# Kernel optimization log

Hardware: AMD Instinct MI355X
Metric: run time of the kernel (lower is better)

The kernel has to match this reference:

```python
import jax, jax.numpy as jnp
import numpy as np

N = 100000
IN_F, C1, C2, C3, OUT_F = 64, 64, 64, 64, 8


def setup_inputs() -> dict:
    key = jax.random.key(0)
    ks = jax.random.split(key, 12)
    x = jax.random.normal(ks[0], (N, IN_F), dtype=jnp.float32)
    edge_index = jax.random.randint(ks[1], (2, 1600000), 0, N, dtype=jnp.int64)

    def lin(kw, kb, fi, fo):
        s = 1.0 / np.sqrt(fi)
        W = jax.random.uniform(kw, (fi, fo), jnp.float32, -s, s)
        b = jax.random.uniform(kb, (fo,), jnp.float32, -s, s)
        return W, b

    W1, b1 = lin(ks[2], ks[3], IN_F, C1)
    W2, b2 = lin(ks[4], ks[5], C1, C2)
    W3, b3 = lin(ks[6], ks[7], C2, C3)
    Wl, bl = lin(ks[8], ks[9], C3, OUT_F)
    return {"x": x, "edge_index": edge_index, "W1": W1, "b1": b1,
            "W2": W2, "b2": b2, "W3": W3, "b3": b3, "Wl": Wl, "bl": bl}


def _gcn_norm(edge_index, n):
    # add self loops, compute symmetric normalization D^-1/2 A D^-1/2
    loops = jnp.arange(n, dtype=edge_index.dtype)
    src = jnp.concatenate([edge_index[0], loops])
    dst = jnp.concatenate([edge_index[1], loops])
    deg = jax.ops.segment_sum(jnp.ones_like(dst, dtype=jnp.float32), dst, num_segments=n)
    dis = jnp.where(deg > 0, jax.lax.rsqrt(deg), 0.0)
    norm = dis[src] * dis[dst]  # [E+N]
    return src, dst, norm


def _gcn_layer(h, W, b, src, dst, norm, n):
    h = h @ W                                   # [N, Fout] small GEMM
    msg = h[src] * norm[:, None]                # gather + scale, [E+N, Fout]
    agg = jax.ops.segment_sum(msg, dst, num_segments=n)  # scatter-add
    return agg + b


def reference(x, edge_index, W1, b1, W2, b2, W3, b3, Wl, bl):
    n = x.shape[0]
    src, dst, norm = _gcn_norm(edge_index, n)
    h = jax.nn.relu(_gcn_layer(x, W1, b1, src, dst, norm, n))
    h = jax.nn.relu(_gcn_layer(h, W2, b2, src, dst, norm, n))
    h = jax.nn.relu(_gcn_layer(h, W3, b3, src, dst, norm, n))
    return h @ Wl + bl
```

## Files before the change

kernel.cpp:

```cpp
#include <hip/hip_runtime.h>
#include <hip/hip_fp16.h>

#define F 64
#define CHUNK 2048
#define BN 512
#define BSHIFT 9
#define CAP 20480

typedef int v4i __attribute__((ext_vector_type(4)));

__device__ __forceinline__ float rlane(float v, int l) {
    return __uint_as_float(__builtin_amdgcn_readlane(__float_as_uint(v), l));
}

__global__ __launch_bounds__(256) void k_blkcnt(const int* __restrict__ dst,
                                                int* __restrict__ blkcnt,
                                                int E, int NB, int NBKT) {
    __shared__ int lcnt[256];
    int b = blockIdx.x, t = threadIdx.x;
    lcnt[t] = 0;
    __syncthreads();
    int e0 = b * CHUNK;
#pragma unroll
    for (int k = 0; k < 8; ++k) {
        int e = e0 + t + k * 256;
        if (e < E) {
            int d = __builtin_nontemporal_load(&dst[e]);
            atomicAdd(&lcnt[d >> BSHIFT], 1);
        }
    }
    __syncthreads();
    if (t < NBKT) blkcnt[t * NB + b] = lcnt[t];
}

__global__ __launch_bounds__(256) void k_bktscan(const int* __restrict__ blkcnt,
                                                 int* __restrict__ blkoff,
                                                 int* __restrict__ bkttot, int NB) {
    __shared__ int s[256];
    __shared__ int running;
    int seg = blockIdx.x;
    int t = threadIdx.x;
    if (t == 0) running = 0;
    __syncthreads();
    for (int base = 0; base < NB; base += 256) {
        int i = base + t;
        int v = (i < NB) ? blkcnt[seg * NB + i] : 0;
        s[t] = v;
        __syncthreads();
        for (int off = 1; off < 256; off <<= 1) {
            int x = (t >= off) ? s[t - off] : 0;
            __syncthreads();
            s[t] += x;
            __syncthreads();
        }
        int rbase = running;
        if (i < NB) blkoff[seg * NB + i] = rbase + s[t] - v;
        int ctot = s[255];
        __syncthreads();
        if (t == 0) running = rbase + ctot;
        __syncthreads();
    }
    if (t == 0) bkttot[seg] = running;
}

__global__ void k_sb(const int* __restrict__ bkttot, int* __restrict__ sb, int NBKT) {
    __shared__ int s[256];
    int t = threadIdx.x;
    int v = (t < NBKT) ? bkttot[t] : 0;
    s[t] = v;
    __syncthreads();
    for (int off = 1; off < 256; off <<= 1) {
        int x = (t >= off) ? s[t - off] : 0;
        __syncthreads();
        s[t] += x;
        __syncthreads();
    }
    if (t < NBKT) sb[t] = s[t] - v;
    if (t == NBKT - 1) sb[NBKT] = s[t];
}

__global__ __launch_bounds__(256) void k_stage2(const int* __restrict__ src,
                                                const int* __restrict__ dst,
                                                const int* __restrict__ blkoff,
                                                const int* __restrict__ sb,
                                                uint2* __restrict__ stage,
                                                int E, int NB, int NBKT) {
    __shared__ int lcnt[256];
    __shared__ int lbase[257];
    __shared__ int obase[256];
    __shared__ int s[256];
    __shared__ uint2 rec[CHUNK];
    __shared__ unsigned char binof[CHUNK];
    int b = blockIdx.x, t = threadIdx.x;
    lcnt[t] = 0;
    __syncthreads();
    int e0 = b * CHUNK;
    int myseg[8], myrank[8];
    uint2 myrec[8];
#pragma unroll
    for (int k = 0; k < 8; ++k) {
        int e = e0 + t + k * 256;
        myseg[k] = -1;
        if (e < E) {
            int d = __builtin_nontemporal_load(&dst[e]);
            int sv = __builtin_nontemporal_load(&src[e]);
            int sg = d >> BSHIFT;
            myseg[k] = sg;
            myrank[k] = atomicAdd(&lcnt[sg], 1);
            myrec[k] = make_uint2((unsigned)d, (unsigned)sv);
        }
    }
    __syncthreads();
    int v = lcnt[t];
    s[t] = v;
    __syncthreads();
    for (int off = 1; off < 256; off <<= 1) {
        int x = (t >= off) ? s[t - off] : 0;
        __syncthreads();
        s[t] += x;
        __syncthreads();
    }
    lbase[t] = s[t] - v;
    if (t == 255) lbase[256] = s[255];
    obase[t] = (t < NBKT) ? sb[t] + blkoff[t * NB + b] : 0;
    __syncthreads();
#pragma unroll
    for (int k = 0; k < 8; ++k) {
        if (myseg[k] >= 0) {
            int p = lbase[myseg[k]] + myrank[k];
            rec[p] = myrec[k];
            binof[p] = (unsigned char)myseg[k];
        }
    }
    __syncthreads();
    int tot = lbase[256];
    for (int j = t; j < tot; j += 256) {
        int sg = binof[j];
        stage[obase[sg] + (j - lbase[sg])] = rec[j];
    }
}

__global__ __launch_bounds__(1024) void k_bincount(const uint2* __restrict__ stage,
                                                   const int* __restrict__ sb,
                                                   int* __restrict__ count, int n) {
    __shared__ int lc[BN];
    int bkt = blockIdx.x, t = threadIdx.x;
    int nb0 = bkt << BSHIFT;
    for (int q = t; q < BN; q += 1024) lc[q] = 0;
    __syncthreads();
    int r0 = sb[bkt], r1 = sb[bkt + 1];
    for (int j = r0 + t; j < r1; j += 1024) {
        uint2 r = stage[j];
        atomicAdd(&lc[(int)r.x - nb0], 1);
    }
    __syncthreads();
    for (int q = t; q < BN; q += 1024) {
        int node = nb0 + q;
        if (node < n) count[node] = lc[q];
    }
}

__global__ void k_reduce(const int* __restrict__ c, int* __restrict__ bsum, int n) {
    __shared__ int s[256];
    int t = threadIdx.x;
    int i = blockIdx.x * 256 + t;
    s[t] = (i < n) ? ((c[i] + 3) & ~3) : 0;
    __syncthreads();
    for (int off = 128; off > 0; off >>= 1) {
        if (t < off) s[t] += s[t + off];
        __syncthreads();
    }
    if (t == 0) bsum[blockIdx.x] = s[0];
}

__global__ void k_scan_bsum(int* bs, int nb) {
    __shared__ int s[512];
    int t = threadIdx.x;
    int v = (t < nb) ? bs[t] : 0;
    s[t] = v;
    __syncthreads();
    for (int off = 1; off < 512; off <<= 1) {
        int x = (t >= off) ? s[t - off] : 0;
        __syncthreads();
        s[t] += x;
        __syncthreads();
    }
    if (t < nb) bs[t] = s[t] - v;
}

__global__ void k_scan_write(const int* __restrict__ c, const int* __restrict__ boff,
                             int* __restrict__ row_start, float* __restrict__ dis, int n) {
    __shared__ int s[256];
    int t = threadIdx.x;
    int i = blockIdx.x * 256 + t;
    int cv = (i < n) ? c[i] : 0;
    int v = (cv + 3) & ~3;
    if (i >= n) v = 0;
    s[t] = v;
    __syncthreads();
    for (int off = 1; off < 256; off <<= 1) {
        int x = (t >= off) ? s[t - off] : 0;
        __syncthreads();
        s[t] += x;
        __syncthreads();
    }
    if (i <= n) {
        row_start[i] = s[t] - v + boff[blockIdx.x];
        if (i < n) dis[i] = rsqrtf((float)(cv + 1));
    }
}

__global__ __launch_bounds__(256) void k_binfill(const uint2* __restrict__ stage,
                                                 const int* __restrict__ sb,
                                                 const int* __restrict__ row_start,
                                                 int* __restrict__ csr, int n) {
    __shared__ int lcur[BN];
    __shared__ int buf[CAP];
    int bkt = blockIdx.x, t = threadIdx.x;
    int nb0 = bkt << BSHIFT;
    int nend = min(nb0 + BN, n);
    int w0 = row_start[nb0];
    int w1 = row_start[nend];
    int wlen = w1 - w0;
    for (int j = t; j < wlen && j < CAP; j += 256) buf[j] = n;
    for (int q = t; q < BN; q += 256) {
        int node = nb0 + q;
        lcur[q] = (node < nend) ? row_start[node] - w0 : 0;
    }
    __syncthreads();
    int r0 = sb[bkt], r1 = sb[bkt + 1];
    for (int j = r0 + t; j < r1; j += 256) {
        uint2 r = stage[j];
        int p = atomicAdd(&lcur[(int)r.x - nb0], 1);
        if (p < CAP) buf[p] = (int)r.y;
    }
    __syncthreads();
    for (int j = t; j < wlen && j < CAP; j += 256) csr[w0 + j] = buf[j];
}

__global__ void k_prep(const float4* __restrict__ x4, const float* __restrict__ dis,
                       uint2* __restrict__ hs, uint2* __restrict__ hs2, int n) {
    int i = blockIdx.x * blockDim.x + threadIdx.x;
    int tot = (n + 1) * 16;
    if (i < tot) {
        int row = i >> 4;
        float dv = 0.0f;
        float4 v = make_float4(0.f, 0.f, 0.f, 0.f);
        if (row < n) { dv = dis[row]; v = x4[i]; }
        __half2 h01 = __floats2half2_rn(dv * v.x, dv * v.y);
        __half2 h23 = __floats2half2_rn(dv * v.z, dv * v.w);
        uint2 u;
        u.x = *(unsigned*)&h01;
        u.y = *(unsigned*)&h23;
        hs[i] = u;
    } else if (i < tot + 16) {
        hs2[(size_t)n * 16 + (i - tot)] = make_uint2(0u, 0u);
    }
}

__device__ __forceinline__ void h4acc(uint2 u, float* t) {
    float2 fa = __half22float2(*(__half2*)&u.x);
    float2 fb = __half22float2(*(__half2*)&u.y);
    t[0] += fa.x; t[1] += fa.y; t[2] += fb.x; t[3] += fb.y;
}

__global__ __launch_bounds__(256) void k_layer(const __half* __restrict__ hin,
                                               const float* __restrict__ W,
                                               const float* __restrict__ b,
                                               const int* __restrict__ row_start,
                                               const int* __restrict__ csr,
                                               const float* __restrict__ dis,
                                               __half* __restrict__ hout,
                                               int n, int scale_out) {
    __shared__ float Ws[F * F];
    int tid = threadIdx.x;
#pragma unroll
    for (int i = 0; i < 16; ++i) Ws[tid + i * 256] = W[tid + i * 256];
    __syncthreads();
    int lane = tid & 63;
    int g = lane >> 4;
    int sub = lane & 15;
    int r0 = (blockIdx.x * 4 + (tid >> 6)) * 4;
    if (r0 >= n) return;

    int s0 = row_start[r0];
    int s1 = row_start[r0 + 1];
    int s2 = row_start[r0 + 2];
    int s3 = row_start[r0 + 3];
    int s4 = row_start[r0 + 4];

    float a0[4] = {0, 0, 0, 0};
    float a1[4] = {0, 0, 0, 0};
    float a2[4] = {0, 0, 0, 0};
    float a3[4] = {0, 0, 0, 0};

    const v4i* csr4 = (const v4i*)csr;
    const uint2* h2 = (const uint2*)hin;
    int B0 = s0 >> 2, B4 = s4 >> 2;

    auto ldidx = [&](int bb) -> v4i {
        int mybb = bb + g;
        bool valid = mybb < B4;
        v4i qq = __builtin_nontemporal_load(csr4 + (valid ? mybb : B0));
        if (!valid) { qq.x = n; qq.y = n; qq.z = n; qq.w = n; }
        return qq;
    };

    if (B0 < B4) {
        v4i qcur = ldidx(B0);
        v4i qnxt = (B0 + 4 < B4) ? ldidx(B0 + 4) : qcur;
        uint2 Gc0 = h2[((size_t)qcur.x << 4) + sub];
        uint2 Gc1 = h2[((size_t)qcur.y << 4) + sub];
        uint2 Gc2 = h2[((size_t)qcur.z << 4) + sub];
        uint2 Gc3 = h2[((size_t)qcur.w << 4) + sub];

        for (int bb = B0; bb < B4; bb += 4) {
            bool hasn = bb + 4 < B4;
            uint2 Gn0, Gn1, Gn2, Gn3;
            if (hasn) {
                Gn0 = h2[((size_t)qnxt.x << 4) + sub];
                Gn1 = h2[((size_t)qnxt.y << 4) + sub];
                Gn2 = h2[((size_t)qnxt.z << 4) + sub];
                Gn3 = h2[((size_t)qnxt.w << 4) + sub];
            }
            v4i qn2 = (bb + 8 < B4) ? ldidx(bb + 8) : qnxt;

            int slot = (bb + g) << 2;
            int r = (slot >= s1) + ((slot >= s2) + (slot >= s3));
            float t[4] = {0, 0, 0, 0};
            h4acc(Gc0, t); h4acc(Gc1, t); h4acc(Gc2, t); h4acc(Gc3, t);
            float m0 = (r == 0) ? 1.0f : 0.0f;
            float m1 = (r == 1) ? 1.0f : 0.0f;
            float m2 = (r == 2) ? 1.0f : 0.0f;
            float m3 = (r == 3) ? 1.0f : 0.0f;
#pragma unroll
            for (int m = 0; m < 4; ++m) {
                a0[m] = fmaf(m0, t[m], a0[m]);
                a1[m] = fmaf(m1, t[m], a1[m]);
                a2[m] = fmaf(m2, t[m], a2[m]);
                a3[m] = fmaf(m3, t[m], a3[m]);
            }
            qnxt = qn2;
            if (hasn) { Gc0 = Gn0; Gc1 = Gn1; Gc2 = Gn2; Gc3 = Gn3; }
        }
    }

#pragma unroll
    for (int m = 0; m < 4; ++m) {
        a0[m] += __shfl_xor(a0[m], 16); a0[m] += __shfl_xor(a0[m], 32);
        a1[m] += __shfl_xor(a1[m], 16); a1[m] += __shfl_xor(a1[m], 32);
        a2[m] += __shfl_xor(a2[m], 16); a2[m] += __shfl_xor(a2[m], 32);
        a3[m] += __shfl_xor(a3[m], 16); a3[m] += __shfl_xor(a3[m], 32);
    }

    {
        uint2 u0 = h2[((size_t)(r0 + 0) << 4) + sub];
        uint2 u1 = h2[((size_t)(r0 + 1) << 4) + sub];
        uint2 u2 = h2[((size_t)(r0 + 2) << 4) + sub];
        uint2 u3 = h2[((size_t)(r0 + 3) << 4) + sub];
        h4acc(u0, a0); h4acc(u1, a1); h4acc(u2, a2); h4acc(u3, a3);
    }
    float d0 = dis[r0 + 0], d1 = dis[r0 + 1], d2 = dis[r0 + 2], d3 = dis[r0 + 3];
#pragma unroll
    for (int m = 0; m < 4; ++m) {
        a0[m] *= d0; a1[m] *= d1; a2[m] *= d2; a3[m] *= d3;
    }

    float bb_ = b[lane];
    float y0 = bb_, y1 = bb_, y2 = bb_, y3 = bb_;
#pragma unroll
    for (int a = 0; a < 16; ++a) {
#pragma unroll
        for (int m = 0; m < 4; ++m) {
            float w = Ws[(((a << 2) + m) << 6) + lane];
            y0 = fmaf(rlane(a0[m], a), w, y0);
            y1 = fmaf(rlane(a1[m], a), w, y1);
            y2 = fmaf(rlane(a2[m], a), w, y2);
            y3 = fmaf(rlane(a3[m], a), w, y3);
        }
    }
    y0 = fmaxf(y0, 0.0f);
    y1 = fmaxf(y1, 0.0f);
    y2 = fmaxf(y2, 0.0f);
    y3 = fmaxf(y3, 0.0f);
    if (scale_out) { y0 *= d0; y1 *= d1; y2 *= d2; y3 *= d3; }
    hout[((size_t)(r0 + 0) << 6) + lane] = __float2half(y0);
    hout[((size_t)(r0 + 1) << 6) + lane] = __float2half(y1);
    hout[((size_t)(r0 + 2) << 6) + lane] = __float2half(y2);
    hout[((size_t)(r0 + 3) << 6) + lane] = __float2half(y3);
}

__global__ __launch_bounds__(256) void k_final(const __half* __restrict__ h,
                                               const float* __restrict__ Wl,
                                               const float* __restrict__ bl,
                                               float* __restrict__ out, int n) {
    __shared__ float Ws[F * 8];
    __shared__ float bs[8];
    int tid = threadIdx.x;
    Ws[tid] = Wl[tid];
    Ws[tid + 256] = Wl[tid + 256];
    if (tid < 8) bs[tid] = bl[tid];
    __syncthreads();
    int idx = blockIdx.x * 256 + tid;
    if (idx >= n * 8) return;
    int row = idx >> 3;
    int o = idx & 7;
    const __half* hr = h + (size_t)row * F;
    float acc = bs[o];
#pragma unroll
    for (int k = 0; k < F; ++k) acc = fmaf(__half2float(hr[k]), Ws[k * 8 + o], acc);
    out[idx] = acc;
}

extern "C" void kernel_launch(void* const* d_in, const int* in_sizes, int n_in,
                              void* d_out, int out_size, void* d_ws, size_t ws_size,
                              hipStream_t stream) {
    const float* x  = (const float*)d_in[0];
    const int*   ei = (const int*)d_in[1];
    const float* W1 = (const float*)d_in[2];
    const float* b1 = (const float*)d_in[3];
    const float* W2 = (const float*)d_in[4];
    const float* b2 = (const float*)d_in[5];
    const float* W3 = (const float*)d_in[6];
    const float* b3 = (const float*)d_in[7];
    const float* Wl = (const float*)d_in[8];
    const float* bl = (const float*)d_in[9];
    float* out = (float*)d_out;

    int n = in_sizes[0] / F;
    int E = in_sizes[1] / 2;
    const int* src = ei;
    const int* dst = ei + E;

    int np   = (n + 256) & ~255;
    int nb   = (np + 255) / 256;
    int cap  = E + 3 * n + 64;
    int NB   = (E + CHUNK - 1) / CHUNK;
    int NBKT = (n + BN - 1) >> BSHIFT;

    int*    count     = (int*)d_ws;
    int*    row_start = count + np;
    int*    bsum      = row_start + np;
    int*    blkcnt    = bsum + 512;
    int*    blkoff    = blkcnt + 256 * NB;
    int*    bkttot    = blkoff + 256 * NB;
    int*    sb        = bkttot + 256;
    float*  dis       = (float*)(sb + 272);
    uint2*  stage     = (uint2*)(dis + np);
    int*    csr       = (int*)(stage + E);
    __half* buf1      = (__half*)(csr + ((cap + 3) & ~3));
    __half* buf2      = buf1 + (size_t)(n + 1) * F;

    k_blkcnt<<<NB, 256, 0, stream>>>(dst, blkcnt, E, NB, NBKT);

    k_bktscan<<<NBKT, 256, 0, stream>>>(blkcnt, blkoff, bkttot, NB);
    k_sb<<<1, 256, 0, stream>>>(bkttot, sb, NBKT);
    k_stage2<<<NB, 256, 0, stream>>>(src, dst, blkoff, sb, stage, E, NB, NBKT);

    k_bincount<<<NBKT, 1024, 0, stream>>>(stage, sb, count, n);

    k_reduce<<<nb, 256, 0, stream>>>(count, bsum, n);
    k_scan_bsum<<<1, 512, 0, stream>>>(bsum, nb);
    k_scan_write<<<nb, 256, 0, stream>>>(count, bsum, row_start, dis, n);

    k_binfill<<<NBKT, 256, 0, stream>>>(stage, sb, row_start, csr, n);

    k_prep<<<((n + 1) * 16 + 16 + 255) / 256, 256, 0, stream>>>(
        (const float4*)x, dis, (uint2*)buf1, (uint2*)buf2, n);

    int nb_l = (n / 4 + 3) / 4;
    k_layer<<<nb_l, 256, 0, stream>>>(buf1, W1, b1, row_start, csr, dis, buf2, n, 1);
    k_layer<<<nb_l, 256, 0, stream>>>(buf2, W2, b2, row_start, csr, dis, buf1, n, 1);
    k_layer<<<nb_l, 256, 0, stream>>>(buf1, W3, b3, row_start, csr, dis, buf2, n, 0);

    k_final<<<(n * 8 + 255) / 256, 256, 0, stream>>>(buf2, Wl, bl, out, n);
}
```

Baseline: 317.0 us.

## Pack staged edges into 32-bit records and deepen the gather prefetch pipeline

Staged edge records shrink from a uint2 of (dst, src) to one 32-bit word that holds the local destination offset in the high bits and a 17-bit source index in the low bits. This halves the staging traffic in stage2, bincount and binfill. The aggregation loop now prefetches feature rows two index groups ahead instead of one, using a three-deep register rotation to hide gather latency. The packing assumes n < 2^17 and bucket offsets under 512, and the deeper prefetch raises register pressure and may cost occupancy.

```diff
diff --git a/kernel.cpp b/kernel.cpp
--- a/kernel.cpp
+++ b/kernel.cpp
@@ -83,20 +83,20 @@
                                                 const int* __restrict__ dst,
                                                 const int* __restrict__ blkoff,
                                                 const int* __restrict__ sb,
-                                                uint2* __restrict__ stage,
+                                                unsigned* __restrict__ stage,
                                                 int E, int NB, int NBKT) {
     __shared__ int lcnt[256];
     __shared__ int lbase[257];
     __shared__ int obase[256];
     __shared__ int s[256];
-    __shared__ uint2 rec[CHUNK];
+    __shared__ unsigned rec[CHUNK];
     __shared__ unsigned char binof[CHUNK];
     int b = blockIdx.x, t = threadIdx.x;
     lcnt[t] = 0;
     __syncthreads();
     int e0 = b * CHUNK;
     int myseg[8], myrank[8];
-    uint2 myrec[8];
+    unsigned myrec[8];
 #pragma unroll
     for (int k = 0; k < 8; ++k) {
         int e = e0 + t + k * 256;
@@ -107,7 +107,7 @@
             int sg = d >> BSHIFT;
             myseg[k] = sg;
             myrank[k] = atomicAdd(&lcnt[sg], 1);
-            myrec[k] = make_uint2((unsigned)d, (unsigned)sv);
+            myrec[k] = ((unsigned)(d & (BN - 1)) << 17) | (unsigned)sv;
         }
     }
     __syncthreads();
@@ -140,7 +140,7 @@
     }
 }
 
-__global__ __launch_bounds__(1024) void k_bincount(const uint2* __restrict__ stage,
+__global__ __launch_bounds__(1024) void k_bincount(const unsigned* __restrict__ stage,
                                                    const int* __restrict__ sb,
                                                    int* __restrict__ count, int n) {
     __shared__ int lc[BN];
@@ -150,8 +150,8 @@
     __syncthreads();
     int r0 = sb[bkt], r1 = sb[bkt + 1];
     for (int j = r0 + t; j < r1; j += 1024) {
-        uint2 r = stage[j];
-        atomicAdd(&lc[(int)r.x - nb0], 1);
+        unsigned r = stage[j];
+        atomicAdd(&lc[r >> 17], 1);
     }
     __syncthreads();
     for (int q = t; q < BN; q += 1024) {
@@ -210,7 +210,7 @@
     }
 }
 
-__global__ __launch_bounds__(256) void k_binfill(const uint2* __restrict__ stage,
+__global__ __launch_bounds__(256) void k_binfill(const unsigned* __restrict__ stage,
                                                  const int* __restrict__ sb,
                                                  const int* __restrict__ row_start,
                                                  int* __restrict__ csr, int n) {
@@ -230,9 +230,9 @@
     __syncthreads();
     int r0 = sb[bkt], r1 = sb[bkt + 1];
     for (int j = r0 + t; j < r1; j += 256) {
-        uint2 r = stage[j];
-        int p = atomicAdd(&lcur[(int)r.x - nb0], 1);
-        if (p < CAP) buf[p] = (int)r.y;
+        unsigned r = stage[j];
+        int p = atomicAdd(&lcur[r >> 17], 1);
+        if (p < CAP) buf[p] = (int)(r & 0x1FFFFu);
     }
     __syncthreads();
     for (int j = t; j < wlen && j < CAP; j += 256) csr[w0 + j] = buf[j];
@@ -307,28 +307,29 @@
     };
 
     if (B0 < B4) {
-        v4i qcur = ldidx(B0);
-        v4i qnxt = (B0 + 4 < B4) ? ldidx(B0 + 4) : qcur;
-        uint2 Gc0 = h2[((size_t)qcur.x << 4) + sub];
-        uint2 Gc1 = h2[((size_t)qcur.y << 4) + sub];
-        uint2 Gc2 = h2[((size_t)qcur.z << 4) + sub];
-        uint2 Gc3 = h2[((size_t)qcur.w << 4) + sub];
+        v4i qA = ldidx(B0);
+        v4i qB = ldidx(B0 + 4);
+        v4i qC = ldidx(B0 + 8);
+        uint2 GA0 = h2[((size_t)qA.x << 4) + sub];
+        uint2 GA1 = h2[((size_t)qA.y << 4) + sub];
+        uint2 GA2 = h2[((size_t)qA.z << 4) + sub];
+        uint2 GA3 = h2[((size_t)qA.w << 4) + sub];
+        uint2 GB0 = h2[((size_t)qB.x << 4) + sub];
+        uint2 GB1 = h2[((size_t)qB.y << 4) + sub];
+        uint2 GB2 = h2[((size_t)qB.z << 4) + sub];
+        uint2 GB3 = h2[((size_t)qB.w << 4) + sub];
 
         for (int bb = B0; bb < B4; bb += 4) {
-            bool hasn = bb + 4 < B4;
-            uint2 Gn0, Gn1, Gn2, Gn3;
-            if (hasn) {
-                Gn0 = h2[((size_t)qnxt.x << 4) + sub];
-                Gn1 = h2[((size_t)qnxt.y << 4) + sub];
-                Gn2 = h2[((size_t)qnxt.z << 4) + sub];
-                Gn3 = h2[((size_t)qnxt.w << 4) + sub];
-            }
-            v4i qn2 = (bb + 8 < B4) ? ldidx(bb + 8) : qnxt;
+            uint2 GC0 = h2[((size_t)qC.x << 4) + sub];
+            uint2 GC1 = h2[((size_t)qC.y << 4) + sub];
+            uint2 GC2 = h2[((size_t)qC.z << 4) + sub];
+            uint2 GC3 = h2[((size_t)qC.w << 4) + sub];
+            v4i qD = ldidx(bb + 12);
 
             int slot = (bb + g) << 2;
             int r = (slot >= s1) + ((slot >= s2) + (slot >= s3));
             float t[4] = {0, 0, 0, 0};
-            h4acc(Gc0, t); h4acc(Gc1, t); h4acc(Gc2, t); h4acc(Gc3, t);
+            h4acc(GA0, t); h4acc(GA1, t); h4acc(GA2, t); h4acc(GA3, t);
             float m0 = (r == 0) ? 1.0f : 0.0f;
             float m1 = (r == 1) ? 1.0f : 0.0f;
             float m2 = (r == 2) ? 1.0f : 0.0f;
@@ -340,8 +341,9 @@
                 a2[m] = fmaf(m2, t[m], a2[m]);
                 a3[m] = fmaf(m3, t[m], a3[m]);
             }
-            qnxt = qn2;
-            if (hasn) { Gc0 = Gn0; Gc1 = Gn1; Gc2 = Gn2; Gc3 = Gn3; }
+            GA0 = GB0; GA1 = GB1; GA2 = GB2; GA3 = GB3;
+            GB0 = GC0; GB1 = GC1; GB2 = GC2; GB3 = GC3;
+            qC = qD;
         }
     }
 
@@ -438,18 +440,18 @@
     int NB   = (E + CHUNK - 1) / CHUNK;
     int NBKT = (n + BN - 1) >> BSHIFT;
 
-    int*    count     = (int*)d_ws;
-    int*    row_start = count + np;
-    int*    bsum      = row_start + np;
-    int*    blkcnt    = bsum + 512;
-    int*    blkoff    = blkcnt + 256 * NB;
-    int*    bkttot    = blkoff + 256 * NB;
-    int*    sb        = bkttot + 256;
-    float*  dis       = (float*)(sb + 272);
-    uint2*  stage     = (uint2*)(dis + np);
-    int*    csr       = (int*)(stage + E);
-    __half* buf1      = (__half*)(csr + ((cap + 3) & ~3));
-    __half* buf2      = buf1 + (size_t)(n + 1) * F;
+    int*      count     = (int*)d_ws;
+    int*      row_start = count + np;
+    int*      bsum      = row_start + np;
+    int*      blkcnt    = bsum + 512;
+    int*      blkoff    = blkcnt + 256 * NB;
+    int*      bkttot    = blkoff + 256 * NB;
+    int*      sb        = bkttot + 256;
+    float*    dis       = (float*)(sb + 272);
+    unsigned* stage     = (unsigned*)(dis + np);
+    int*      csr       = (int*)(stage + ((E + 3) & ~3));
+    __half*   buf1      = (__half*)(csr + ((cap + 3) & ~3));
+    __half*   buf2      = buf1 + (size_t)(n + 1) * F;
 
     k_blkcnt<<<NB, 256, 0, stream>>>(dst, blkcnt, E, NB, NBKT);
 
```

Result: slower. 348.5 us (+9.9%).
